# Kernel tuning notes

Measured on AMD Instinct MI355X. Metric: run time of the kernel, lower is better.

## Reference

```python
import jax, jax.numpy as jnp
import numpy as np

B, L, H, D = 16, 2048, 768, 768
M, TPL = 8, 16  # labels per example, tokens per label


def setup_inputs() -> dict:
    key = jax.random.key(0)
    k1, k2, k3, k4 = jax.random.split(key, 4)
    hidden_states = jax.random.normal(k1, (B, L, H), dtype=jnp.float32)
    # first M*TPL tokens are label tokens with ids 1..M, rest are text tokens
    pos = jnp.arange(L)
    row = jnp.where(pos < M * TPL, pos // TPL + 1, 0).astype(jnp.int32)
    lmask = jnp.broadcast_to(row, (B, L))
    input_ids = jax.random.randint(k2, (B, L), 0, 30000, dtype=jnp.int32)
    attention_mask = jnp.ones((B, L), dtype=jnp.int32)
    Wt = jax.random.normal(k3, (H, D), dtype=jnp.float32) / np.sqrt(H)
    bt = jnp.zeros((D,), dtype=jnp.float32)
    Wl = jax.random.normal(k4, (H, D), dtype=jnp.float32) / np.sqrt(H)
    bl = jnp.zeros((D,), dtype=jnp.float32)
    attention_temperature = jnp.array(1.0, dtype=jnp.float32)
    logit_scale = jnp.array(2.0, dtype=jnp.float32)
    return dict(hidden_states=hidden_states, Wt=Wt, bt=bt, Wl=Wl, bl=bl,
                attention_temperature=attention_temperature, logit_scale=logit_scale,
                lmask=lmask, input_ids=input_ids, attention_mask=attention_mask,
                num_labels=M)


def reference(hidden_states, Wt, bt, Wl, bl, attention_temperature, logit_scale,
              lmask, input_ids, attention_mask, num_labels):
    # hidden_states: (B, L, H); lmask: (B, L) int label ids (>0 = label token)
    Bb, Ll, _ = hidden_states.shape
    Mm = num_labels  # static python int (== max label id)
    proj_text = hidden_states @ Wt + bt            # (B, L, D)  text_projector (dropout=eval identity)
    proj_label = hidden_states @ Wl + bl           # (B, L, D)  label_projector on all tokens
    label_tok = lmask > 0                          # (B, L)
    # segment-mean of projected label tokens per (batch, label_id) slot
    flat_idx = jnp.where(label_tok,
                         jnp.arange(Bb, dtype=lmask.dtype)[:, None] * Mm + (lmask - 1),
                         Bb * Mm).reshape(-1)
    masked = proj_label * label_tok[..., None].astype(proj_label.dtype)
    seg = jax.ops.segment_sum(masked.reshape(Bb * Ll, -1), flat_idx,
                              num_segments=Bb * Mm + 1)[: Bb * Mm]
    counts = jax.ops.segment_sum(label_tok.reshape(-1).astype(jnp.float32), flat_idx,
                                 num_segments=Bb * Mm + 1)[: Bb * Mm]
    aggregated_labels = seg / jnp.maximum(counts, 1.0)[:, None]   # (B*M, D)
    agg = aggregated_labels.reshape(Bb, Mm, -1)                   # (B, M, D)
    # attention-weighted text pooling per label over text tokens
    text_mask = (lmask == 0) & (attention_mask == 1)              # (B, L)
    temp = jnp.maximum(jnp.abs(attention_temperature), 0.1)
    scores = jnp.einsum('bmd,bld->bml', agg, proj_text) / temp
    scores = jnp.where(text_mask[:, None, :], scores, -jnp.inf)
    attn = jax.nn.softmax(scores, axis=-1)                        # (B, M, L)
    aggregated_text = jnp.einsum('bml,bld->bmd', attn, proj_text).reshape(Bb * Mm, -1)
    # cosine similarity head with learnable temperature exp(logit_scale)
    tn = aggregated_text / jnp.clip(jnp.linalg.norm(aggregated_text, axis=-1, keepdims=True), 1e-8)
    ln = aggregated_labels / jnp.clip(jnp.linalg.norm(aggregated_labels, axis=-1, keepdims=True), 1e-8)
    scale = jnp.exp(logit_scale)
    logits = jnp.sum(tn * ln, axis=-1, keepdims=True) * scale     # (B*M, 1)
    all_batch_ids = jnp.repeat(jnp.arange(Bb), Mm)
    all_label_ids = jnp.tile(jnp.arange(1, Mm + 1), Bb)
    return (logits, all_batch_ids, all_label_ids, aggregated_labels, scale, aggregated_text)
```

## Files before the change

kernel.cpp:

```cpp
#include <hip/hip_runtime.h>
#include <hip/hip_bf16.h>

typedef __attribute__((ext_vector_type(8))) short s16x8;
typedef __attribute__((ext_vector_type(4))) float f32x4;

#define BB 16
#define LL 2048
#define HH 768
#define DD 768
#define MM 8

#define O_LOGITS 0
#define O_BID    128
#define O_LID    256
#define O_AGGL   384
#define O_SCALE  98688
#define O_AGGT   98689

#define WTT_OFF  0u
#define WLT_OFF  1179648u
#define WTB_OFF  2359296u
#define HBAR_OFF 3538944u
#define QH_OFF   3932160u
#define HST_OFF  4325376u
#define CVEC_OFF 4718592u
#define PML_OFF  4719104u
#define PO_OFF   4751872u
#define SK_OFF   17334784u

__device__ __forceinline__ short f2bf(float x) {
  union { float f; unsigned u; } v; v.f = x;
  unsigned r = v.u + 0x7FFFu + ((v.u >> 16) & 1u);
  return (short)(r >> 16);
}

#define GLOAD_LDS16(gp, lp) __builtin_amdgcn_global_load_lds( \
    (const __attribute__((address_space(1))) unsigned int*)(gp), \
    (__attribute__((address_space(3))) unsigned int*)(lp), 16, 0, 0)

__global__ void k_prep(const float* __restrict__ Wt, const float* __restrict__ Wl,
                       short* __restrict__ Wtt, short* __restrict__ Wlt,
                       short* __restrict__ Wtb,
                       const float* __restrict__ hs, const int* __restrict__ lmask,
                       float* __restrict__ hbar) {
  __shared__ float tile[64][65];
  __shared__ int list[LL];
  __shared__ int nlist_s;
  int bx = blockIdx.x;
  int t = threadIdx.x;
  if (bx < 432) {
    int z = bx / 144, r = bx % 144;
    int kb = (r % 12) * 64, nb = (r / 12) * 64;
    int c = t & 63;
    int r0 = (t >> 6) * 16;
    if (z == 2) {
#pragma unroll
      for (int i = 0; i < 16; ++i) {
        int rr = kb + r0 + i;
        Wtb[(size_t)rr * DD + nb + c] = f2bf(Wt[(size_t)rr * DD + nb + c]);
      }
      return;
    }
    const float* src = z ? Wl : Wt;
    short* dst = z ? Wlt : Wtt;
#pragma unroll
    for (int i = 0; i < 16; ++i)
      tile[r0 + i][c] = src[(size_t)(kb + r0 + i) * DD + nb + c];
    __syncthreads();
#pragma unroll
    for (int i = 0; i < 16; ++i)
      dst[(size_t)(nb + r0 + i) * HH + kb + c] = f2bf(tile[c][r0 + i]);
    return;
  }
  int bh = bx - 432;
  int b = bh >> 3, m = bh & 7;
  int lane = t & 63, w = t >> 6;
  if (w == 0) {
    int base = 0;
    for (int win = 0; win < LL / 64; ++win) {
      int l = win * 64 + lane;
      bool match = (lmask[b * LL + l] == m + 1);
      unsigned long long mk = __ballot(match);
      if (match) {
        int pos = base + (int)__popcll(mk & ((1ull << lane) - 1ull));
        list[pos] = l;
      }
      base += (int)__popcll(mk);
    }
    if (lane == 0) nlist_s = base;
  }
  __syncthreads();
  int n = nlist_s;
  float inv = 1.0f / (float)(n > 1 ? n : 1);
  float a0 = 0.f, a1 = 0.f, a2 = 0.f;
  for (int i = 0; i < n; ++i) {
    const float* rr = hs + (size_t)(b * LL + list[i]) * HH;
    a0 += rr[t]; a1 += rr[t + 256]; a2 += rr[t + 512];
  }
  float* dst = hbar + (size_t)(b * MM + m) * HH;
  dst[t] = a0 * inv; dst[t + 256] = a1 * inv; dst[t + 512] = a2 * inv;
}

__global__ __launch_bounds__(256, 3)
void k_skgemm(const float* __restrict__ A, const short* __restrict__ Bt,
              float* __restrict__ part) {
  __shared__ short As[128][64];
  __shared__ short Bs[2][128][64];
  int t = threadIdx.x;
  int lane = t & 63, w = t >> 6;
  int wm = w >> 1, wn = w & 1;
  int n0 = blockIdx.x * 128;
  int kt0 = blockIdx.y * 3;

  f32x4 acc[4][4] = {};
  float4 areg[8];

  auto issueA = [&](int kt) {
    const float* Ag = A + (size_t)(kt0 + kt) * 64;
#pragma unroll
    for (int i = 0; i < 8; ++i) {
      int slot = i * 256 + t;
      int row = slot >> 4, c = slot & 15;
      areg[i] = *(const float4*)(Ag + (size_t)row * HH + c * 4);
    }
  };
  auto issueB = [&](int kt, int buf) {
    const short* Bg = Bt + (size_t)n0 * HH + (size_t)(kt0 + kt) * 64;
#pragma unroll
    for (int i = 0; i < 4; ++i) {
      int slot = i * 256 + w * 64 + lane;
      int row = slot >> 3, c = slot & 7;
      int cs = c ^ (row & 7);
      GLOAD_LDS16(Bg + (size_t)row * HH + cs * 8,
                  (char*)&Bs[0][0][0] + (size_t)buf * 16384 + (size_t)(i * 256 + w * 64) * 16);
    }
  };
  auto writeA = [&]() {
#pragma unroll
    for (int i = 0; i < 8; ++i) {
      int slot = i * 256 + t;
      int row = slot >> 4, c = slot & 15;
      unsigned d0, d1;
      asm("v_cvt_pk_bf16_f32 %0, %1, %2" : "=v"(d0) : "v"(areg[i].x), "v"(areg[i].y));
      asm("v_cvt_pk_bf16_f32 %0, %1, %2" : "=v"(d1) : "v"(areg[i].z), "v"(areg[i].w));
      int phys = (c >> 1) ^ (row & 7);
      uint2 val = {d0, d1};
      *(uint2*)((char*)&As[0][0] + (size_t)row * 128 + phys * 16 + (c & 1) * 8) = val;
    }
  };
  auto compute = [&](int buf) {
#pragma unroll
    for (int kk = 0; kk < 2; ++kk) {
      s16x8 a[4], bb[4];
#pragma unroll
      for (int i = 0; i < 4; ++i) {
        int row = wm * 64 + i * 16 + (lane & 15);
        int p = (kk * 4 + (lane >> 4)) ^ (row & 7);
        a[i] = *(const s16x8*)((const char*)&As[0][0] + (size_t)row * 128 + p * 16);
      }
#pragma unroll
      for (int i = 0; i < 4; ++i) {
        int row = wn * 64 + i * 16 + (lane & 15);
        int p = (kk * 4 + (lane >> 4)) ^ (row & 7);
        bb[i] = *(const s16x8*)((const char*)&Bs[0][0][0] + (size_t)buf * 16384 + (size_t)row * 128 + p * 16);
      }
#pragma unroll
      for (int mi = 0; mi < 4; ++mi)
#pragma unroll
        for (int ni = 0; ni < 4; ++ni)
          acc[mi][ni] = __builtin_amdgcn_mfma_f32_16x16x32_bf16(a[mi], bb[ni], acc[mi][ni], 0, 0, 0);
    }
  };

  issueA(0); issueB(0, 0);
  writeA();
  __syncthreads();
  for (int kt = 0; kt < 3; ++kt) {
    if (kt + 1 < 3) { issueA(kt + 1); issueB(kt + 1, (kt + 1) & 1); }
    compute(kt & 1);
    __syncthreads();
    if (kt + 1 < 3) {
      writeA();
      __syncthreads();
    }
  }

  float* po = part + (size_t)blockIdx.y * 128 * HH;
#pragma unroll
  for (int mi = 0; mi < 4; ++mi) {
    int row = wm * 64 + mi * 16 + ((lane >> 4) * 4);
#pragma unroll
    for (int ni = 0; ni < 4; ++ni) {
      int col = n0 + wn * 64 + ni * 16 + (lane & 15);
#pragma unroll
      for (int j = 0; j < 4; ++j)
        po[(size_t)(row + j) * HH + col] = acc[mi][ni][j];
    }
  }
}

__global__ void k_red_agg(const float* __restrict__ part, const float* __restrict__ bl,
                          const float* __restrict__ bt, float* __restrict__ out,
                          float* __restrict__ cvec) {
  int row = blockIdx.x;
  int t = threadIdx.x;
  int lane = t & 63, w = t >> 6;
  __shared__ float wred[4];
  float dotbt = 0.f;
#pragma unroll
  for (int cc = 0; cc < 3; ++cc) {
    int c = cc * 256 + t;
    float s = bl[c];
#pragma unroll
    for (int kc = 0; kc < 4; ++kc)
      s += part[((size_t)kc * 128 + row) * HH + c];
    out[O_AGGL + (size_t)row * DD + c] = s;
    dotbt += s * bt[c];
  }
  for (int sh = 32; sh; sh >>= 1) dotbt += __shfl_xor(dotbt, sh, 64);
  if (lane == 0) wred[w] = dotbt;
  __syncthreads();
  if (t == 0) cvec[row] = wred[0] + wred[1] + wred[2] + wred[3];
}

__global__ void k_red_qh(const float* __restrict__ part, float* __restrict__ qh) {
  int row = blockIdx.x;
  int t = threadIdx.x;
#pragma unroll
  for (int cc = 0; cc < 3; ++cc) {
    int c = cc * 256 + t;
    float s = 0.f;
#pragma unroll
    for (int kc = 0; kc < 4; ++kc)
      s += part[((size_t)kc * 128 + row) * HH + c];
    qh[(size_t)row * HH + c] = s;
  }
}

__global__ __launch_bounds__(256, 3)
void k_attnpool(const float* __restrict__ hs, const float* __restrict__ qh,
                const float* __restrict__ cvec, const int* __restrict__ lmask,
                const int* __restrict__ amask, const float* __restrict__ temp_p,
                float* __restrict__ part_o, float* __restrict__ part_ml) {
  __shared__ short As[4][2][16][64];
  __shared__ short Bs[16][776];
  __shared__ float w_lds[64][8];
  int chunk = blockIdx.x;
  int b = blockIdx.y;
  int t = threadIdx.x;
  int lane = t & 63, w = t >> 6;

  const float* qsrc = qh + (size_t)b * MM * HH;
  for (int c = t; c < HH; c += 256) {
#pragma unroll
    for (int r = 0; r < 8; ++r) Bs[r][c] = f2bf(qsrc[(size_t)r * HH + c]);
#pragma unroll
    for (int r = 8; r < 16; ++r) Bs[r][c] = 0;
  }

  const float* Hg = hs + (size_t)(b * LL + chunk * 64) * HH;
  const float* Wrow = Hg + (size_t)(w * 16) * HH;
  float4 areg[4];
  auto issueA = [&](int kt) {
#pragma unroll
    for (int i = 0; i < 4; ++i) {
      int slot = i * 64 + lane;
      int row = slot >> 4, c = slot & 15;
      areg[i] = *(const float4*)(Wrow + (size_t)row * HH + kt * 64 + c * 4);
    }
  };
  auto writeA = [&](int buf) {
#pragma unroll
    for (int i = 0; i < 4; ++i) {
      int slot = i * 64 + lane;
      int row = slot >> 4, c = slot & 15;
      unsigned d0, d1;
      asm("v_cvt_pk_bf16_f32 %0, %1, %2" : "=v"(d0) : "v"(areg[i].x), "v"(areg[i].y));
      asm("v_cvt_pk_bf16_f32 %0, %1, %2" : "=v"(d1) : "v"(areg[i].z), "v"(areg[i].w));
      int phys = (c >> 1) ^ (row & 7);
      uint2 val = {d0, d1};
      *(uint2*)((char*)&As[w][buf][0][0] + (size_t)row * 128 + phys * 16 + (c & 1) * 8) = val;
    }
  };

  f32x4 acc = {};
  issueA(0);
  writeA(0);
  __syncthreads();
  for (int kt = 0; kt < 12; ++kt) {
    if (kt + 1 < 12) issueA(kt + 1);
    int buf = kt & 1;
#pragma unroll
    for (int kk = 0; kk < 2; ++kk) {
      int r = lane & 15;
      int p = (kk * 4 + (lane >> 4)) ^ (r & 7);
      s16x8 a = *(const s16x8*)((const char*)&As[w][buf][0][0] + (size_t)r * 128 + p * 16);
      s16x8 bfr = *(const s16x8*)&Bs[lane & 15][kt * 64 + kk * 32 + (lane >> 4) * 8];
      acc = __builtin_amdgcn_mfma_f32_16x16x32_bf16(a, bfr, acc, 0, 0, 0);
    }
    if (kt + 1 < 12) writeA(buf ^ 1);
  }

  float inv_temp = 1.0f / fmaxf(fabsf(temp_p[0]), 0.1f);
  int m = lane & 15;
  int tok0 = w * 16 + (lane >> 4) * 4;
  if (m < MM) {
    float cv = cvec[b * MM + m];
    int4 lm = *(const int4*)&lmask[b * LL + chunk * 64 + tok0];
    int4 am = *(const int4*)&amask[b * LL + chunk * 64 + tok0];
    w_lds[tok0 + 0][m] = (lm.x == 0 && am.x == 1) ? (acc[0] + cv) * inv_temp : -1e30f;
    w_lds[tok0 + 1][m] = (lm.y == 0 && am.y == 1) ? (acc[1] + cv) * inv_temp : -1e30f;
    w_lds[tok0 + 2][m] = (lm.z == 0 && am.z == 1) ? (acc[2] + cv) * inv_temp : -1e30f;
    w_lds[tok0 + 3][m] = (lm.w == 0 && am.w == 1) ? (acc[3] + cv) * inv_temp : -1e30f;
  }
  __syncthreads();

#pragma unroll
  for (int half = 0; half < 2; ++half) {
    int mm = w + half * 4;
    float v = w_lds[lane][mm];
    float mx = v;
    for (int s = 32; s; s >>= 1) mx = fmaxf(mx, __shfl_xor(mx, s, 64));
    float e = __expf(v - mx);
    float l = e;
    for (int s = 32; s; s >>= 1) l += __shfl_xor(l, s, 64);
    w_lds[lane][mm] = e;
    if (lane == 0) {
      float* pml = part_ml + ((size_t)(chunk * BB + b) * MM + mm) * 2;
      pml[0] = mx; pml[1] = l;
    }
  }
  __syncthreads();

  if (t < 192) {
    int h0 = t * 4;
    f32x4 o[8] = {};
    const float* hp = Hg + h0;
    for (int tok = 0; tok < 64; ++tok) {
      float4 hv = *(const float4*)(hp + (size_t)tok * HH);
      float4 w0 = *(const float4*)&w_lds[tok][0];
      float4 w1 = *(const float4*)&w_lds[tok][4];
      o[0][0] += w0.x * hv.x; o[0][1] += w0.x * hv.y; o[0][2] += w0.x * hv.z; o[0][3] += w0.x * hv.w;
      o[1][0] += w0.y * hv.x; o[1][1] += w0.y * hv.y; o[1][2] += w0.y * hv.z; o[1][3] += w0.y * hv.w;
      o[2][0] += w0.z * hv.x; o[2][1] += w0.z * hv.y; o[2][2] += w0.z * hv.z; o[2][3] += w0.z * hv.w;
      o[3][0] += w0.w * hv.x; o[3][1] += w0.w * hv.y; o[3][2] += w0.w * hv.z; o[3][3] += w0.w * hv.w;
      o[4][0] += w1.x * hv.x; o[4][1] += w1.x * hv.y; o[4][2] += w1.x * hv.z; o[4][3] += w1.x * hv.w;
      o[5][0] += w1.y * hv.x; o[5][1] += w1.y * hv.y; o[5][2] += w1.y * hv.z; o[5][3] += w1.y * hv.w;
      o[6][0] += w1.z * hv.x; o[6][1] += w1.z * hv.y; o[6][2] += w1.z * hv.z; o[6][3] += w1.z * hv.w;
      o[7][0] += w1.w * hv.x; o[7][1] += w1.w * hv.y; o[7][2] += w1.w * hv.z; o[7][3] += w1.w * hv.w;
    }
    float* po = part_o + (size_t)(chunk * BB + b) * MM * HH + h0;
#pragma unroll
    for (int mm = 0; mm < 8; ++mm)
      *(f32x4*)(po + (size_t)mm * HH) = o[mm];
  }
}

__global__ void k_finish(const float* __restrict__ part_o, const float* __restrict__ part_ml,
                         float* __restrict__ hst) {
  int row = blockIdx.x;
  int b = row >> 3, m = row & 7;
  int t = threadIdx.x;
  float mg = -1e30f;
#pragma unroll
  for (int lc = 0; lc < 32; ++lc)
    mg = fmaxf(mg, part_ml[((size_t)(lc * BB + b) * MM + m) * 2]);
  float L = 0.f;
  f32x4 acc = {};
  int h0 = t * 4;
  for (int lc = 0; lc < 32; ++lc) {
    const float* pml = part_ml + ((size_t)(lc * BB + b) * MM + m) * 2;
    float f = __expf(pml[0] - mg);
    L += pml[1] * f;
    f32x4 v = *(const f32x4*)(part_o + ((size_t)(lc * BB + b) * MM + m) * HH + h0);
    acc[0] += v[0] * f; acc[1] += v[1] * f; acc[2] += v[2] * f; acc[3] += v[3] * f;
  }
  float inv = 1.0f / L;
  f32x4 r = {acc[0] * inv, acc[1] * inv, acc[2] * inv, acc[3] * inv};
  *(f32x4*)(hst + (size_t)row * HH + h0) = r;
}

__global__ void k_head(const float* __restrict__ part, const float* __restrict__ bt,
                       const float* __restrict__ lscale_p, float* __restrict__ out) {
  int row = blockIdx.x;
  int lane = threadIdx.x;
  const float* al = out + O_AGGL + (size_t)row * DD;
  float dot = 0.f, nt = 0.f, nl = 0.f;
  for (int i = lane; i < DD; i += 64) {
    float a = bt[i];
#pragma unroll
    for (int kc = 0; kc < 4; ++kc)
      a += part[((size_t)kc * 128 + row) * HH + i];
    out[O_AGGT + (size_t)row * DD + i] = a;
    float c = al[i];
    dot += a * c; nt += a * a; nl += c * c;
  }
  for (int s = 32; s; s >>= 1) {
    dot += __shfl_xor(dot, s, 64);
    nt  += __shfl_xor(nt, s, 64);
    nl  += __shfl_xor(nl, s, 64);
  }
  if (lane == 0) {
    float scale = expf(lscale_p[0]);
    float denom = fmaxf(sqrtf(nt), 1e-8f) * fmaxf(sqrtf(nl), 1e-8f);
    out[O_LOGITS + row] = dot / denom * scale;
    out[O_BID + row] = (float)(row >> 3);
    out[O_LID + row] = (float)((row & 7) + 1);
    if (row == 0) out[O_SCALE] = scale;
  }
}

extern "C" void kernel_launch(void* const* d_in, const int* in_sizes, int n_in,
                              void* d_out, int out_size, void* d_ws, size_t ws_size,
                              hipStream_t stream) {
  const float* hs    = (const float*)d_in[0];
  const float* Wt    = (const float*)d_in[1];
  const float* bt    = (const float*)d_in[2];
  const float* Wl    = (const float*)d_in[3];
  const float* bl    = (const float*)d_in[4];
  const float* atemp = (const float*)d_in[5];
  const float* lsc   = (const float*)d_in[6];
  const int*   lmask = (const int*)d_in[7];
  const int*   amask = (const int*)d_in[9];
  float* out = (float*)d_out;
  char* ws = (char*)d_ws;
  short* Wtt  = (short*)(ws + WTT_OFF);
  short* Wlt  = (short*)(ws + WLT_OFF);
  short* Wtb  = (short*)(ws + WTB_OFF);
  float* hbar = (float*)(ws + HBAR_OFF);
  float* qh   = (float*)(ws + QH_OFF);
  float* hst  = (float*)(ws + HST_OFF);
  float* cvec = (float*)(ws + CVEC_OFF);
  float* pml  = (float*)(ws + PML_OFF);
  float* po   = (float*)(ws + PO_OFF);
  float* skp  = (float*)(ws + SK_OFF);

  k_prep<<<560, 256, 0, stream>>>(Wt, Wl, Wtt, Wlt, Wtb, hs, lmask, hbar);
  k_skgemm<<<dim3(6, 4), 256, 0, stream>>>(hbar, Wlt, skp);
  k_red_agg<<<128, 256, 0, stream>>>(skp, bl, bt, out, cvec);
  k_skgemm<<<dim3(6, 4), 256, 0, stream>>>(out + O_AGGL, Wtb, skp);
  k_red_qh<<<128, 256, 0, stream>>>(skp, qh);
  k_attnpool<<<dim3(32, 16), 256, 0, stream>>>(hs, qh, cvec, lmask, amask, atemp, po, pml);
  k_finish<<<128, 192, 0, stream>>>(po, pml, hst);
  k_skgemm<<<dim3(6, 4), 256, 0, stream>>>(hst, Wtt, skp);
  k_head<<<128, 64, 0, stream>>>(skp, bt, lsc, out);
}
```

Before: 85.63 us.

## Fuse qh split-K reduction into attnpool and split its K loop across 512 threads

```diff
diff --git a/kernel.cpp b/kernel.cpp
--- a/kernel.cpp
+++ b/kernel.cpp
@@ -223,60 +223,57 @@
   if (t == 0) cvec[row] = wred[0] + wred[1] + wred[2] + wred[3];
 }
 
-__global__ void k_red_qh(const float* __restrict__ part, float* __restrict__ qh) {
-  int row = blockIdx.x;
-  int t = threadIdx.x;
-#pragma unroll
-  for (int cc = 0; cc < 3; ++cc) {
-    int c = cc * 256 + t;
-    float s = 0.f;
-#pragma unroll
-    for (int kc = 0; kc < 4; ++kc)
-      s += part[((size_t)kc * 128 + row) * HH + c];
-    qh[(size_t)row * HH + c] = s;
-  }
-}
-
-__global__ __launch_bounds__(256, 3)
-void k_attnpool(const float* __restrict__ hs, const float* __restrict__ qh,
+__global__ __launch_bounds__(512, 4)
+void k_attnpool(const float* __restrict__ hs, const float* __restrict__ qhp,
                 const float* __restrict__ cvec, const int* __restrict__ lmask,
                 const int* __restrict__ amask, const float* __restrict__ temp_p,
                 float* __restrict__ part_o, float* __restrict__ part_ml) {
-  __shared__ short As[4][2][16][64];
+  __shared__ short As[8][2][16][64];
   __shared__ short Bs[16][776];
+  __shared__ float w_acc[4][64][4];
   __shared__ float w_lds[64][8];
   int chunk = blockIdx.x;
   int b = blockIdx.y;
   int t = threadIdx.x;
   int lane = t & 63, w = t >> 6;
-
-  const float* qsrc = qh + (size_t)b * MM * HH;
-  for (int c = t; c < HH; c += 256) {
-#pragma unroll
-    for (int r = 0; r < 8; ++r) Bs[r][c] = f2bf(qsrc[(size_t)r * HH + c]);
+  int wq = w & 3, kw = w >> 2;
+
+  for (int c = t; c < HH; c += 512) {
+#pragma unroll
+    for (int r = 0; r < 8; ++r) {
+      size_t o = (size_t)(b * MM + r) * HH + c;
+      float s = qhp[o] + qhp[(size_t)128 * HH + o] + qhp[(size_t)256 * HH + o] + qhp[(size_t)384 * HH + o];
+      Bs[r][c] = f2bf(s);
+    }
 #pragma unroll
     for (int r = 8; r < 16; ++r) Bs[r][c] = 0;
   }
 
   const float* Hg = hs + (size_t)(b * LL + chunk * 64) * HH;
-  const float* Wrow = Hg + (size_t)(w * 16) * HH;
-  float4 areg[4];
-  auto issueA = [&](int kt) {
+  const float* Wrow = Hg + (size_t)(wq * 16) * HH;
+  int kbase = kw * 384;
+  float4 areg[2][4];
+
+  auto issueA = [&](int set, int kt) {
 #pragma unroll
     for (int i = 0; i < 4; ++i) {
       int slot = i * 64 + lane;
       int row = slot >> 4, c = slot & 15;
-      areg[i] = *(const float4*)(Wrow + (size_t)row * HH + kt * 64 + c * 4);
-    }
-  };
-  auto writeA = [&](int buf) {
+      if (set == 0)
+        areg[0][i] = *(const float4*)(Wrow + (size_t)row * HH + kbase + kt * 64 + c * 4);
+      else
+        areg[1][i] = *(const float4*)(Wrow + (size_t)row * HH + kbase + kt * 64 + c * 4);
+    }
+  };
+  auto writeA = [&](int set, int buf) {
 #pragma unroll
     for (int i = 0; i < 4; ++i) {
       int slot = i * 64 + lane;
       int row = slot >> 4, c = slot & 15;
+      float4 v = set == 0 ? areg[0][i] : areg[1][i];
       unsigned d0, d1;
-      asm("v_cvt_pk_bf16_f32 %0, %1, %2" : "=v"(d0) : "v"(areg[i].x), "v"(areg[i].y));
-      asm("v_cvt_pk_bf16_f32 %0, %1, %2" : "=v"(d1) : "v"(areg[i].z), "v"(areg[i].w));
+      asm("v_cvt_pk_bf16_f32 %0, %1, %2" : "=v"(d0) : "v"(v.x), "v"(v.y));
+      asm("v_cvt_pk_bf16_f32 %0, %1, %2" : "=v"(d1) : "v"(v.z), "v"(v.w));
       int phys = (c >> 1) ^ (row & 7);
       uint2 val = {d0, d1};
       *(uint2*)((char*)&As[w][buf][0][0] + (size_t)row * 128 + phys * 16 + (c & 1) * 8) = val;
@@ -284,27 +281,38 @@
   };
 
   f32x4 acc = {};
-  issueA(0);
-  writeA(0);
-  __syncthreads();
-  for (int kt = 0; kt < 12; ++kt) {
-    if (kt + 1 < 12) issueA(kt + 1);
+  issueA(0, 0); issueA(1, 1);
+  writeA(0, 0);
+  __syncthreads();
+#pragma unroll
+  for (int kt = 0; kt < 6; ++kt) {
     int buf = kt & 1;
 #pragma unroll
     for (int kk = 0; kk < 2; ++kk) {
       int r = lane & 15;
       int p = (kk * 4 + (lane >> 4)) ^ (r & 7);
       s16x8 a = *(const s16x8*)((const char*)&As[w][buf][0][0] + (size_t)r * 128 + p * 16);
-      s16x8 bfr = *(const s16x8*)&Bs[lane & 15][kt * 64 + kk * 32 + (lane >> 4) * 8];
+      s16x8 bfr = *(const s16x8*)&Bs[lane & 15][kbase + kt * 64 + kk * 32 + (lane >> 4) * 8];
       acc = __builtin_amdgcn_mfma_f32_16x16x32_bf16(a, bfr, acc, 0, 0, 0);
     }
-    if (kt + 1 < 12) writeA(buf ^ 1);
+    if (kt + 1 < 6) writeA((kt + 1) & 1, (kt + 1) & 1);
+    if (kt + 2 < 6) issueA(kt & 1, kt + 2);
+  }
+
+  if (kw == 1) {
+    w_acc[wq][lane][0] = acc[0]; w_acc[wq][lane][1] = acc[1];
+    w_acc[wq][lane][2] = acc[2]; w_acc[wq][lane][3] = acc[3];
+  }
+  __syncthreads();
+  if (kw == 0) {
+    acc[0] += w_acc[wq][lane][0]; acc[1] += w_acc[wq][lane][1];
+    acc[2] += w_acc[wq][lane][2]; acc[3] += w_acc[wq][lane][3];
   }
 
   float inv_temp = 1.0f / fmaxf(fabsf(temp_p[0]), 0.1f);
   int m = lane & 15;
-  int tok0 = w * 16 + (lane >> 4) * 4;
-  if (m < MM) {
+  int tok0 = wq * 16 + (lane >> 4) * 4;
+  if (kw == 0 && m < MM) {
     float cv = cvec[b * MM + m];
     int4 lm = *(const int4*)&lmask[b * LL + chunk * 64 + tok0];
     int4 am = *(const int4*)&amask[b * LL + chunk * 64 + tok0];
@@ -315,44 +323,42 @@
   }
   __syncthreads();
 
-#pragma unroll
-  for (int half = 0; half < 2; ++half) {
-    int mm = w + half * 4;
-    float v = w_lds[lane][mm];
+  {
+    float v = w_lds[lane][w];
     float mx = v;
     for (int s = 32; s; s >>= 1) mx = fmaxf(mx, __shfl_xor(mx, s, 64));
     float e = __expf(v - mx);
     float l = e;
     for (int s = 32; s; s >>= 1) l += __shfl_xor(l, s, 64);
-    w_lds[lane][mm] = e;
+    w_lds[lane][w] = e;
     if (lane == 0) {
-      float* pml = part_ml + ((size_t)(chunk * BB + b) * MM + mm) * 2;
+      float* pml = part_ml + ((size_t)(chunk * BB + b) * MM + w) * 2;
       pml[0] = mx; pml[1] = l;
     }
   }
   __syncthreads();
 
-  if (t < 192) {
-    int h0 = t * 4;
-    f32x4 o[8] = {};
+  if (t < 384) {
+    int h0 = t * 2;
+    float2 o[8] = {};
     const float* hp = Hg + h0;
     for (int tok = 0; tok < 64; ++tok) {
-      float4 hv = *(const float4*)(hp + (size_t)tok * HH);
+      float2 hv = *(const float2*)(hp + (size_t)tok * HH);
       float4 w0 = *(const float4*)&w_lds[tok][0];
       float4 w1 = *(const float4*)&w_lds[tok][4];
-      o[0][0] += w0.x * hv.x; o[0][1] += w0.x * hv.y; o[0][2] += w0.x * hv.z; o[0][3] += w0.x * hv.w;
-      o[1][0] += w0.y * hv.x; o[1][1] += w0.y * hv.y; o[1][2] += w0.y * hv.z; o[1][3] += w0.y * hv.w;
-      o[2][0] += w0.z * hv.x; o[2][1] += w0.z * hv.y; o[2][2] += w0.z * hv.z; o[2][3] += w0.z * hv.w;
-      o[3][0] += w0.w * hv.x; o[3][1] += w0.w * hv.y; o[3][2] += w0.w * hv.z; o[3][3] += w0.w * hv.w;
-      o[4][0] += w1.x * hv.x; o[4][1] += w1.x * hv.y; o[4][2] += w1.x * hv.z; o[4][3] += w1.x * hv.w;
-      o[5][0] += w1.y * hv.x; o[5][1] += w1.y * hv.y; o[5][2] += w1.y * hv.z; o[5][3] += w1.y * hv.w;
-      o[6][0] += w1.z * hv.x; o[6][1] += w1.z * hv.y; o[6][2] += w1.z * hv.z; o[6][3] += w1.z * hv.w;
-      o[7][0] += w1.w * hv.x; o[7][1] += w1.w * hv.y; o[7][2] += w1.w * hv.z; o[7][3] += w1.w * hv.w;
+      o[0].x += w0.x * hv.x; o[0].y += w0.x * hv.y;
+      o[1].x += w0.y * hv.x; o[1].y += w0.y * hv.y;
+      o[2].x += w0.z * hv.x; o[2].y += w0.z * hv.y;
+      o[3].x += w0.w * hv.x; o[3].y += w0.w * hv.y;
+      o[4].x += w1.x * hv.x; o[4].y += w1.x * hv.y;
+      o[5].x += w1.y * hv.x; o[5].y += w1.y * hv.y;
+      o[6].x += w1.z * hv.x; o[6].y += w1.z * hv.y;
+      o[7].x += w1.w * hv.x; o[7].y += w1.w * hv.y;
     }
     float* po = part_o + (size_t)(chunk * BB + b) * MM * HH + h0;
 #pragma unroll
     for (int mm = 0; mm < 8; ++mm)
-      *(f32x4*)(po + (size_t)mm * HH) = o[mm];
+      *(float2*)(po + (size_t)mm * HH) = o[mm];
   }
 }
 
@@ -428,7 +434,6 @@
   short* Wlt  = (short*)(ws + WLT_OFF);
   short* Wtb  = (short*)(ws + WTB_OFF);
   float* hbar = (float*)(ws + HBAR_OFF);
-  float* qh   = (float*)(ws + QH_OFF);
   float* hst  = (float*)(ws + HST_OFF);
   float* cvec = (float*)(ws + CVEC_OFF);
   float* pml  = (float*)(ws + PML_OFF);
@@ -439,8 +444,7 @@
   k_skgemm<<<dim3(6, 4), 256, 0, stream>>>(hbar, Wlt, skp);
   k_red_agg<<<128, 256, 0, stream>>>(skp, bl, bt, out, cvec);
   k_skgemm<<<dim3(6, 4), 256, 0, stream>>>(out + O_AGGL, Wtb, skp);
-  k_red_qh<<<128, 256, 0, stream>>>(skp, qh);
-  k_attnpool<<<dim3(32, 16), 256, 0, stream>>>(hs, qh, cvec, lmask, amask, atemp, po, pml);
+  k_attnpool<<<dim3(32, 16), 512, 0, stream>>>(hs, skp, cvec, lmask, amask, atemp, po, pml);
   k_finish<<<128, 192, 0, stream>>>(po, pml, hst);
   k_skgemm<<<dim3(6, 4), 256, 0, stream>>>(hst, Wtt, skp);
   k_head<<<128, 64, 0, stream>>>(skp, bt, lsc, out);
```

Measured after the change: 84.47 us. Within noise of the previous version (-1.4%).
